# Performance work log

Measured on AMD Instinct MI355X. Metric: run time of the kernel, lower is better.

The kernel has to match this reference:

```python
import jax, jax.numpy as jnp
import numpy as np

NUM_EMBEDDINGS = 8192
EMBEDDING_DIM = 128


def setup_inputs() -> dict:
    key = jax.random.key(0)
    k1, k2 = jax.random.split(key)
    inputs = jax.random.normal(k1, (8, 32, 32, EMBEDDING_DIM), dtype=jnp.float32)
    embedding_weight = jax.random.normal(k2, (NUM_EMBEDDINGS, EMBEDDING_DIM), dtype=jnp.float32)
    return {"inputs": inputs, "embedding_weight": embedding_weight}


def reference(inputs, embedding_weight):
    # inputs: [B, H, W, C] channels-last; embedding_weight: [K, C]
    input_shape = inputs.shape
    flat_input = inputs.reshape(-1, EMBEDDING_DIM)  # [N, C]

    distances = (
        jnp.sum(flat_input ** 2, axis=1, keepdims=True)
        + jnp.sum(embedding_weight ** 2, axis=1)
        - 2.0 * flat_input @ embedding_weight.T
    )
    encoding_indices = jnp.argmin(distances, axis=1)  # [N]

    # one-hot encodings (returned by the original module)
    encodings = jax.nn.one_hot(encoding_indices, NUM_EMBEDDINGS, dtype=jnp.float32)  # [N, K]

    # quantized via direct gather (same math as one_hot @ weight, no big matmul)
    quantized = embedding_weight[encoding_indices].reshape(input_shape)  # [B,H,W,C]

    # straight-through estimator
    quantized = inputs + jax.lax.stop_gradient(quantized - inputs)

    quantized_nchw = jnp.transpose(quantized, (0, 3, 1, 2))  # [B,C,H,W]
    return quantized_nchw, encodings
```

## Files before the change

kernel.cpp:

```cpp
#include <hip/hip_runtime.h>

typedef _Float16 f16x4 __attribute__((ext_vector_type(4)));
typedef _Float16 f16x8 __attribute__((ext_vector_type(8)));
typedef float    f32x16 __attribute__((ext_vector_type(16)));

#define HN_OFF   0u
#define BEST_OFF 32768u
#define EFH_OFF  98304u
#define EFL_OFF  (98304u + 2097152u)
#define XRH_OFF  (98304u + 2u * 2097152u)
#define XRL_OFF  (98304u + 3u * 2097152u)

#define OUT_ENC  1048576

__global__ __launch_bounds__(256) void k1_convert(const float* __restrict__ x,
                                                  const float* __restrict__ e,
                                                  char* __restrict__ wsb) {
    int bx = blockIdx.x, tid = threadIdx.x;
    if (bx < 64) {
        __shared__ f16x8 lds[4096];
        const float* src = e + (size_t)bx * 16384;
        float* hnp = (float*)(wsb + HN_OFF);
        #pragma unroll
        for (int it = 0; it < 8; it++) {
            int g = it * 256 + tid;
            int row = g >> 4, c16 = g & 15;
            float4 v0 = *(const float4*)(src + row * 128 + c16 * 8);
            float4 v1 = *(const float4*)(src + row * 128 + c16 * 8 + 4);
            float f[8] = {v0.x, v0.y, v0.z, v0.w, v1.x, v1.y, v1.z, v1.w};
            f16x8 hi, lo;
            float ss = 0.f;
            #pragma unroll
            for (int j = 0; j < 8; j++) {
                hi[j] = (_Float16)f[j];
                lo[j] = (_Float16)((f[j] - (float)hi[j]) * 2048.0f);
                ss += f[j] * f[j];
            }
            int sw = row ^ c16;
            lds[c16 * 128 + sw] = hi;
            lds[2048 + c16 * 128 + sw] = lo;
            #pragma unroll
            for (int o = 8; o > 0; o >>= 1) ss += __shfl_down(ss, o, 16);
            if ((tid & 15) == 0) hnp[bx * 128 + row] = 0.5f * ss;
        }
        __syncthreads();
        _Float16* eh = (_Float16*)(wsb + EFH_OFF);
        _Float16* el = (_Float16*)(wsb + EFL_OFF);
        #pragma unroll
        for (int it = 0; it < 16; it++) {
            int g = it * 256 + tid;
            int plane = g >> 11, gg = g & 2047;
            int chunk = gg >> 7, code = gg & 127;
            f16x8 v = lds[plane * 2048 + chunk * 128 + (code ^ chunk)];
            _Float16* dst = plane ? el : eh;
            *(f16x8*)(dst + ((size_t)bx * 2048 + gg) * 8) = v;
        }
    } else {
        int sec = bx - 64;
        size_t off = (size_t)sec * 1024 + tid * 4;
        float4 v = *(const float4*)(x + off);
        f16x4 hi, lo;
        hi[0] = (_Float16)v.x; hi[1] = (_Float16)v.y;
        hi[2] = (_Float16)v.z; hi[3] = (_Float16)v.w;
        lo[0] = (_Float16)((v.x - (float)hi[0]) * 2048.0f);
        lo[1] = (_Float16)((v.y - (float)hi[1]) * 2048.0f);
        lo[2] = (_Float16)((v.z - (float)hi[2]) * 2048.0f);
        lo[3] = (_Float16)((v.w - (float)hi[3]) * 2048.0f);
        *(f16x4*)((_Float16*)(wsb + XRH_OFF) + off) = hi;
        *(f16x4*)((_Float16*)(wsb + XRL_OFF) + off) = lo;
        if (sec < 32)
            ((unsigned long long*)(wsb + BEST_OFF))[sec * 256 + tid] = 0ull;
    }
}

__global__ __launch_bounds__(256, 2) void k2_mfma(char* __restrict__ wsb,
                                                  float* __restrict__ out) {
    const _Float16* xrh = (const _Float16*)(wsb + XRH_OFF);
    const _Float16* xrl = (const _Float16*)(wsb + XRL_OFF);
    const f16x8* efh = (const f16x8*)(wsb + EFH_OFF);
    const f16x8* efl = (const f16x8*)(wsb + EFL_OFF);
    const float* hn = (const float*)(wsb + HN_OFF);
    unsigned long long* bestg = (unsigned long long*)(wsb + BEST_OFF);

    int tid = threadIdx.x;
    int lane = tid & 63, wave = tid >> 6;
    int col = lane & 31, half = lane >> 5;
    int bx = blockIdx.x, by = blockIdx.y;
    int r0 = bx * 128;
    int k0g = by * 1024;
    int row = r0 + wave * 32 + col;

    f16x8 ah[8], al[8];
    #pragma unroll
    for (int s = 0; s < 8; s++) {
        ah[s] = *(const f16x8*)(xrh + (size_t)row * 128 + s * 16 + half * 8);
        al[s] = *(const f16x8*)(xrl + (size_t)row * 128 + s * 16 + half * 8);
    }

    float best[16];
    int bidx[16];
    #pragma unroll
    for (int i = 0; i < 16; i++) { best[i] = -3.0e38f; bidx[i] = 0; }

    float4* enc4 = (float4*)(out + OUT_ENC);
    long zb = (long)(by * 64 + bx) * 32768;
    float4 z4 = make_float4(0.f, 0.f, 0.f, 0.f);

    for (int kt = 0; kt < 8; kt++) {
        const f16x8* ebh = efh + ((size_t)(by * 8 + kt) * 2048 + half * 128 + col);
        const f16x8* ebl = efl + ((size_t)(by * 8 + kt) * 2048 + half * 128 + col);
        #pragma unroll
        for (int sub = 0; sub < 4; sub++) {
            float hnv = hn[k0g + kt * 128 + sub * 32 + col];
            f32x16 a0, a1, a2;
            #pragma unroll
            for (int i = 0; i < 16; i++) { a0[i] = 0.f; a1[i] = 0.f; a2[i] = 0.f; }
            #pragma unroll
            for (int s = 0; s < 8; s++) {
                f16x8 bh = ebh[s * 256 + sub * 32];
                f16x8 bl = ebl[s * 256 + sub * 32];
                a0 = __builtin_amdgcn_mfma_f32_32x32x16_f16(ah[s], bh, a0, 0, 0, 0);
                a1 = __builtin_amdgcn_mfma_f32_32x32x16_f16(ah[s], bl, a1, 0, 0, 0);
                a2 = __builtin_amdgcn_mfma_f32_32x32x16_f16(al[s], bh, a2, 0, 0, 0);
            }
            int code = k0g + kt * 128 + sub * 32 + col;
            #pragma unroll
            for (int r = 0; r < 16; r++) {
                float sc = a0[r] + (a1[r] + a2[r]) * (1.0f / 2048.0f) - hnv;
                if (sc > best[r]) { best[r] = sc; bidx[r] = code; }
            }
        }
        #pragma unroll
        for (int i = 0; i < 16; i++) enc4[zb + kt * 4096 + i * 256 + tid] = z4;
    }

    #pragma unroll
    for (int r = 0; r < 16; r++) {
        float s = best[r];
        int bi = bidx[r];
        #pragma unroll
        for (int m = 1; m < 32; m <<= 1) {
            float qs = __shfl_xor(s, m, 64);
            int qi = __shfl_xor(bi, m, 64);
            if (qs > s || (qs == s && qi < bi)) { s = qs; bi = qi; }
        }
        if (col == 0) {
            int rl = (r & 3) + 8 * (r >> 2) + 4 * half;
            unsigned ub = __float_as_uint(s);
            ub = ((int)ub < 0) ? ~ub : (ub | 0x80000000u);
            unsigned long long p = ((unsigned long long)ub << 32) |
                                   (unsigned long long)(0xFFFFFFFFu - (unsigned)bi);
            atomicMax(&bestg[r0 + wave * 32 + rl], p);
        }
    }
}

__global__ __launch_bounds__(256) void k3_final(const char* __restrict__ wsb,
                                                const float* __restrict__ wgt,
                                                float* __restrict__ out) {
    int n = blockIdx.x * 256 + threadIdx.x;
    unsigned long long p = ((const unsigned long long*)(wsb + BEST_OFF))[n];
    int bi = (int)(0xFFFFFFFFu - (unsigned)(p & 0xFFFFFFFFull));

    out[(size_t)OUT_ENC + (size_t)n * 8192 + bi] = 1.0f;

    int bq = n >> 10, hw = n & 1023;
    float* o = out + (size_t)bq * 131072 + hw;
    const float4* wrow = (const float4*)(wgt + (size_t)bi * 128);
    #pragma unroll
    for (int c4 = 0; c4 < 32; c4++) {
        float4 v = wrow[c4];
        o[(c4 * 4 + 0) * 1024] = v.x;
        o[(c4 * 4 + 1) * 1024] = v.y;
        o[(c4 * 4 + 2) * 1024] = v.z;
        o[(c4 * 4 + 3) * 1024] = v.w;
    }
}

extern "C" void kernel_launch(void* const* d_in, const int* in_sizes, int n_in,
                              void* d_out, int out_size, void* d_ws, size_t ws_size,
                              hipStream_t stream) {
    const float* x = (const float*)d_in[0];
    const float* e = (const float*)d_in[1];
    float* out = (float*)d_out;
    char* ws = (char*)d_ws;

    k1_convert<<<1088, 256, 0, stream>>>(x, e, ws);
    k2_mfma<<<dim3(64, 8), 256, 0, stream>>>(ws, out);
    k3_final<<<32, 256, 0, stream>>>(ws, e, out);
}
```

Measured before the change: 349.7 us.

## Stage codebook tiles in LDS and move encoding zero-fill into convert kernel

```diff
diff --git a/kernel.cpp b/kernel.cpp
--- a/kernel.cpp
+++ b/kernel.cpp
@@ -15,8 +15,17 @@
 
 __global__ __launch_bounds__(256) void k1_convert(const float* __restrict__ x,
                                                   const float* __restrict__ e,
-                                                  char* __restrict__ wsb) {
+                                                  char* __restrict__ wsb,
+                                                  float* __restrict__ out) {
     int bx = blockIdx.x, tid = threadIdx.x;
+    if (bx >= 1088) {
+        int f = bx - 1088;
+        float4* enc4 = (float4*)(out + OUT_ENC) + (size_t)f * 32768;
+        float4 z4 = make_float4(0.f, 0.f, 0.f, 0.f);
+        #pragma unroll
+        for (int i = 0; i < 128; i++) enc4[i * 256 + tid] = z4;
+        return;
+    }
     if (bx < 64) {
         __shared__ f16x8 lds[4096];
         const float* src = e + (size_t)bx * 16384;
@@ -73,12 +82,15 @@
     }
 }
 
-__global__ __launch_bounds__(256, 2) void k2_mfma(char* __restrict__ wsb,
-                                                  float* __restrict__ out) {
+__global__ __launch_bounds__(256, 2) void k2_mfma(char* __restrict__ wsb) {
+    __shared__ _Float16 lds_eh[128 * 128];
+    __shared__ _Float16 lds_el[128 * 128];
+    __shared__ float    lds_hn[1024];
+
     const _Float16* xrh = (const _Float16*)(wsb + XRH_OFF);
     const _Float16* xrl = (const _Float16*)(wsb + XRL_OFF);
-    const f16x8* efh = (const f16x8*)(wsb + EFH_OFF);
-    const f16x8* efl = (const f16x8*)(wsb + EFL_OFF);
+    const _Float16* erh = (const _Float16*)(wsb + EFH_OFF);
+    const _Float16* erl = (const _Float16*)(wsb + EFL_OFF);
     const float* hn = (const float*)(wsb + HN_OFF);
     unsigned long long* bestg = (unsigned long long*)(wsb + BEST_OFF);
 
@@ -97,41 +109,51 @@
         al[s] = *(const f16x8*)(xrl + (size_t)row * 128 + s * 16 + half * 8);
     }
 
+    *(float4*)(lds_hn + tid * 4) = *(const float4*)(hn + k0g + tid * 4);
+
     float best[16];
     int bidx[16];
     #pragma unroll
     for (int i = 0; i < 16; i++) { best[i] = -3.0e38f; bidx[i] = 0; }
 
-    float4* enc4 = (float4*)(out + OUT_ENC);
-    long zb = (long)(by * 64 + bx) * 32768;
-    float4 z4 = make_float4(0.f, 0.f, 0.f, 0.f);
-
     for (int kt = 0; kt < 8; kt++) {
-        const f16x8* ebh = efh + ((size_t)(by * 8 + kt) * 2048 + half * 128 + col);
-        const f16x8* ebl = efl + ((size_t)(by * 8 + kt) * 2048 + half * 128 + col);
+        __syncthreads();
+        const f16x8* sh = (const f16x8*)erh + ((size_t)(by * 8 + kt) * 2048);
+        const f16x8* sl = (const f16x8*)erl + ((size_t)(by * 8 + kt) * 2048);
+        #pragma unroll
+        for (int i = 0; i < 16; i++) {
+            int g = tid + i * 256;
+            int gg = g & 2047;
+            int chunk = gg >> 7, code = gg & 127;
+            f16x8 v = (i < 8) ? sh[gg] : sl[gg];
+            _Float16* dstp = (i < 8) ? lds_eh : lds_el;
+            *(f16x8*)(dstp + code * 128 + ((chunk ^ (code & 15)) * 8)) = v;
+        }
+        __syncthreads();
+
         #pragma unroll
         for (int sub = 0; sub < 4; sub++) {
-            float hnv = hn[k0g + kt * 128 + sub * 32 + col];
             f32x16 a0, a1, a2;
             #pragma unroll
             for (int i = 0; i < 16; i++) { a0[i] = 0.f; a1[i] = 0.f; a2[i] = 0.f; }
+            int cbase = (sub * 32 + col) * 128;
             #pragma unroll
             for (int s = 0; s < 8; s++) {
-                f16x8 bh = ebh[s * 256 + sub * 32];
-                f16x8 bl = ebl[s * 256 + sub * 32];
+                int so = ((s * 2 + half) ^ (col & 15)) * 8;
+                f16x8 bh = *(const f16x8*)(lds_eh + cbase + so);
+                f16x8 bl = *(const f16x8*)(lds_el + cbase + so);
                 a0 = __builtin_amdgcn_mfma_f32_32x32x16_f16(ah[s], bh, a0, 0, 0, 0);
                 a1 = __builtin_amdgcn_mfma_f32_32x32x16_f16(ah[s], bl, a1, 0, 0, 0);
                 a2 = __builtin_amdgcn_mfma_f32_32x32x16_f16(al[s], bh, a2, 0, 0, 0);
             }
             int code = k0g + kt * 128 + sub * 32 + col;
+            float hnv = lds_hn[kt * 128 + sub * 32 + col];
             #pragma unroll
             for (int r = 0; r < 16; r++) {
                 float sc = a0[r] + (a1[r] + a2[r]) * (1.0f / 2048.0f) - hnv;
                 if (sc > best[r]) { best[r] = sc; bidx[r] = code; }
             }
         }
-        #pragma unroll
-        for (int i = 0; i < 16; i++) enc4[zb + kt * 4096 + i * 256 + tid] = z4;
     }
 
     #pragma unroll
@@ -185,7 +207,7 @@
     float* out = (float*)d_out;
     char* ws = (char*)d_ws;
 
-    k1_convert<<<1088, 256, 0, stream>>>(x, e, ws);
-    k2_mfma<<<dim3(64, 8), 256, 0, stream>>>(ws, out);
+    k1_convert<<<1600, 256, 0, stream>>>(x, e, ws, out);
+    k2_mfma<<<dim3(64, 8), 256, 0, stream>>>(ws);
     k3_final<<<32, 256, 0, stream>>>(ws, e, out);
 }
```

Measured after the change: 362.4 us. 1.04x slower.
